# Kernel optimization log

Hardware: AMD Instinct MI355X
Metric: run time of the kernel (lower is better)

## Reference

```python
import jax, jax.numpy as jnp
import numpy as np

ATTN_MULT = 8.0
NEG_INF = float('-inf')

N, Q, S, D = 16, 2048, 2048, 64


def setup_inputs() -> dict:
    key = jax.random.key(0)
    kq, kk, kv, kp = jax.random.split(key, 4)
    return {
        "queries_nqd": jax.random.normal(kq, (N, Q, D), dtype=jnp.float32),
        "keys_nsd": jax.random.normal(kk, (N, S, D), dtype=jnp.float32),
        "values_nsv": jax.random.normal(kv, (N, S, D), dtype=jnp.float32),
        "prefix_len_n": jax.random.randint(kp, (N,), 0, S, dtype=jnp.int64 if jax.config.jax_enable_x64 else jnp.int32),
    }


def reference(queries_nqd, keys_nsd, values_nsv, prefix_len_n):
    # attention_type == 'block_diagonal', backend == 'torch', dropout p == 0
    n, q, d = queries_nqd.shape
    s = keys_nsd.shape[1]
    scale = ATTN_MULT / d
    # prefix-block mask: key position < prefix_len (broadcast over queries)
    block_mask_n1s = (jnp.arange(s)[None, None, :] < prefix_len_n[:, None, None])  # [n,1,s]
    diag_mask_qs = jnp.arange(q)[:, None] == jnp.arange(s)[None, :]                # [q,s]
    mask_nqs = block_mask_n1s | diag_mask_qs[None, :, :]                           # [n,q,s]
    scores_nqs = jnp.einsum('nqd,nsd->nqs', queries_nqd, keys_nsd) * scale
    scores_nqs = jnp.where(mask_nqs, scores_nqs, NEG_INF)
    probs_nqs = jax.nn.softmax(scores_nqs, axis=-1)
    return jnp.einsum('nqs,nsv->nqv', probs_nqs, values_nsv)
```

## Files before the change

### kernel.cpp

```cpp
#include <hip/hip_runtime.h>
#include <hip/hip_bf16.h>
#include <math.h>

#define NH 16
#define QL 2048
#define SL 2048
#define DD 64
#define BQ 128
#define NSPLIT 2
#define PSTR 72
#define QK_SCALE_LOG2E 0.1803368801111f

typedef __attribute__((ext_vector_type(8))) short short8;
typedef __attribute__((ext_vector_type(4))) float floatx4;
typedef __attribute__((ext_vector_type(4))) unsigned short ushort4v;
typedef __attribute__((ext_vector_type(8))) unsigned short ushort8v;

__device__ __forceinline__ unsigned short f2bf(float x) {
    unsigned u = __float_as_uint(x);
    u += 0x7FFFu + ((u >> 16) & 1u);
    return (unsigned short)(u >> 16);
}
__device__ __forceinline__ unsigned int f2bf2u(float x, float y) {
    __hip_bfloat162 h = __float22bfloat162_rn(make_float2(x, y));
    return *(unsigned int*)&h;
}
__device__ __forceinline__ float bf2f(unsigned short h) {
    return __uint_as_float((unsigned)h << 16);
}

__device__ __forceinline__ void gld16(const unsigned short* g, unsigned short* l) {
    __builtin_amdgcn_global_load_lds(
        (const __attribute__((address_space(1))) unsigned int*)g,
        (__attribute__((address_space(3))) unsigned int*)l, 16, 0, 0);
}

__global__ __launch_bounds__(512) void k_prep(
    const float* __restrict__ Kf, const float* __restrict__ Vf,
    unsigned short* __restrict__ Kb, unsigned short* __restrict__ Vtb)
{
    __shared__ unsigned short sT[64][PSTR];
    const int bx = (int)blockIdx.x, tid = (int)threadIdx.x;

    const int gidx = bx * 512 + tid;
    #pragma unroll
    for (int k = 0; k < 2; ++k) {
        int idx = gidx + k * (512 * 512);
        float4 v = ((const float4*)Kf)[idx];
        ushort4v h = { f2bf(v.x), f2bf(v.y), f2bf(v.z), f2bf(v.w) };
        *(ushort4v*)(Kb + (size_t)idx * 4) = h;
    }

    const int n = bx >> 5, s0 = (bx & 31) * 64;
    const float* vb = Vf + ((size_t)n * SL + s0) * DD;
    #pragma unroll
    for (int i = 0; i < 2; ++i) {
        int idx = tid + i * 512;
        int r = idx >> 4, c = (idx & 15) << 2;
        float4 v = *(const float4*)(vb + r * DD + c);
        sT[c + 0][r] = f2bf(v.x);
        sT[c + 1][r] = f2bf(v.y);
        sT[c + 2][r] = f2bf(v.z);
        sT[c + 3][r] = f2bf(v.w);
    }
    __syncthreads();
    const int d = tid >> 3, sg = tid & 7;
    unsigned short* out = Vtb + (size_t)n * DD * SL + (size_t)d * SL + s0 + sg * 8;
    ushort8v a;
    #pragma unroll
    for (int i = 0; i < 8; ++i) a[i] = sT[d][sg * 8 + i];
    *(ushort8v*)out = a;
}

__global__ __launch_bounds__(512, 4) void k_attn(
    const float* __restrict__ Qf, const unsigned short* __restrict__ Kb,
    const unsigned short* __restrict__ Vtb, const int* __restrict__ plen_g,
    unsigned short* __restrict__ Opb, float* __restrict__ Lp)
{
    __shared__ unsigned short sK[4][64 * 64];
    __shared__ unsigned short sVt[4][64 * 64];
    __shared__ unsigned short sP[8 * 16 * 64];

    const int flat = (int)blockIdx.x;
    const int sp   = flat >> 8;
    const int rb   = flat & 255;
    const int n    = (rb + sp) & (NH - 1);
    const int qt   = rb >> 4;
    const int q0   = qt * BQ;
    const int plen = plen_g[n];

    const int tid  = (int)threadIdx.x;
    const int wave = tid >> 6, lane = tid & 63, quad = lane >> 4, l16 = lane & 15;

    const int ptiles = (plen + 63) >> 6;
    const int d0     = q0 >> 6;
    const int tdiag  = d0 + sp;
    const int cnt_p  = (ptiles + 1 - sp) >> 1;
    const int total  = cnt_p + (tdiag >= ptiles ? 1 : 0);

    const int qrow  = wave * 16 + l16;
    const int qglob = q0 + qrow;
    const int pmask = (l16 & 7) * 8;

    const unsigned short* kh = Kb  + (size_t)n * SL * DD;
    const unsigned short* vh = Vtb + (size_t)n * DD * SL;

    const int srow = wave * 8 + (lane >> 3);
    const int scol = ((lane & 7) ^ (srow & 7)) * 8;

    auto tile_of = [&](int i) -> int {
        return (i < cnt_p) ? (sp + (i << 1)) : tdiag;
    };
    auto stage = [&](int t, int b) {
        const unsigned short* kg = kh + ((size_t)t << 6) * DD;
        const unsigned short* vg = vh + (t << 6);
        gld16(kg + srow * DD + scol, sK[b] + wave * 512);
        gld16(vg + (size_t)srow * SL + scol, sVt[b] + wave * 512);
    };

    short8 bQ0, bQ1;
    {
        const float* qf = Qf + ((size_t)(n * QL + qglob)) * DD + quad * 8;
        float4 a0 = *(const float4*)(qf);
        float4 a1 = *(const float4*)(qf + 4);
        float4 c0 = *(const float4*)(qf + 32);
        float4 c1 = *(const float4*)(qf + 36);
        const float S = QK_SCALE_LOG2E;
        unsigned int u0[4] = {
            f2bf2u(a0.x * S, a0.y * S), f2bf2u(a0.z * S, a0.w * S),
            f2bf2u(a1.x * S, a1.y * S), f2bf2u(a1.z * S, a1.w * S) };
        unsigned int u1[4] = {
            f2bf2u(c0.x * S, c0.y * S), f2bf2u(c0.z * S, c0.w * S),
            f2bf2u(c1.x * S, c1.y * S), f2bf2u(c1.z * S, c1.w * S) };
        bQ0 = *(short8*)u0;
        bQ1 = *(short8*)u1;
    }

    stage(tile_of(0), 0);
    if (1 < total) stage(tile_of(1), 1);

    floatx4 acc[4];
    #pragma unroll
    for (int dt = 0; dt < 4; ++dt) acc[dt] = (floatx4){0.f, 0.f, 0.f, 0.f};
    float lsum = 0.f;
    unsigned short* pw = sP + qrow * 64;

    auto do_tile = [&](int t, const unsigned short* sk, const unsigned short* sv) {
        const int s0 = t << 6;

        floatx4 sf[4];
        #pragma unroll
        for (int st2 = 0; st2 < 4; ++st2) sf[st2] = (floatx4){0.f, 0.f, 0.f, 0.f};
        __builtin_amdgcn_s_setprio(1);
        #pragma unroll
        for (int st2 = 0; st2 < 4; ++st2) {
            int krow = st2 * 16 + l16;
            short8 aK0 = *(const short8*)(sk + krow * 64 + (((0 * 4 + quad) ^ (krow & 7)) * 8));
            short8 aK1 = *(const short8*)(sk + krow * 64 + (((1 * 4 + quad) ^ (krow & 7)) * 8));
            sf[st2] = __builtin_amdgcn_mfma_f32_16x16x32_bf16(aK0, bQ0, sf[st2], 0, 0, 0);
            sf[st2] = __builtin_amdgcn_mfma_f32_16x16x32_bf16(aK1, bQ1, sf[st2], 0, 0, 0);
        }
        __builtin_amdgcn_s_setprio(0);

        if (s0 + 64 <= plen) {
            #pragma unroll
            for (int st2 = 0; st2 < 4; ++st2) {
                float p0 = __builtin_amdgcn_exp2f(sf[st2][0]);
                float p1 = __builtin_amdgcn_exp2f(sf[st2][1]);
                float p2 = __builtin_amdgcn_exp2f(sf[st2][2]);
                float p3 = __builtin_amdgcn_exp2f(sf[st2][3]);
                lsum += (p0 + p1) + (p2 + p3);
                uint2 pk = { f2bf2u(p0, p1), f2bf2u(p2, p3) };
                *(uint2*)(pw + ((st2 * 16 + quad * 4) ^ pmask)) = pk;
            }
        } else {
            #pragma unroll
            for (int st2 = 0; st2 < 4; ++st2) {
                float p[4];
                #pragma unroll
                for (int r2 = 0; r2 < 4; ++r2) {
                    int s = s0 + st2 * 16 + quad * 4 + r2;
                    bool valid = (s < plen) || (s == qglob);
                    p[r2] = __builtin_amdgcn_exp2f(valid ? sf[st2][r2] : -INFINITY);
                    lsum += p[r2];
                }
                uint2 pk = { f2bf2u(p[0], p[1]), f2bf2u(p[2], p[3]) };
                *(uint2*)(pw + ((st2 * 16 + quad * 4) ^ pmask)) = pk;
            }
        }

        __builtin_amdgcn_s_setprio(1);
        #pragma unroll
        for (int ks = 0; ks < 2; ++ks) {
            short8 aP = *(const short8*)(pw + ((ks * 32 + quad * 8) ^ pmask));
            #pragma unroll
            for (int dt = 0; dt < 4; ++dt) {
                int vrow = dt * 16 + l16;
                short8 bV = *(const short8*)(sv + vrow * 64 + (((ks * 4 + quad) ^ (vrow & 7)) * 8));
                acc[dt] = __builtin_amdgcn_mfma_f32_16x16x32_bf16(aP, bV, acc[dt], 0, 0, 0);
            }
        }
        __builtin_amdgcn_s_setprio(0);
    };

    const int np = (total + 1) >> 1;
    for (int p = 0; p < np; ++p) {
        asm volatile("s_waitcnt vmcnt(0) lgkmcnt(0)" ::: "memory");
        __builtin_amdgcn_s_barrier();

        const int i0 = 2 * p;
        const int nb = 2 * ((p + 1) & 1);
        if (i0 + 2 < total) stage(tile_of(i0 + 2), nb);
        if (i0 + 3 < total) stage(tile_of(i0 + 3), nb + 1);

        const int cb = 2 * (p & 1);
        do_tile(tile_of(i0), sK[cb], sVt[cb]);
        if (i0 + 1 < total)
            do_tile(tile_of(i0 + 1), sK[cb + 1], sVt[cb + 1]);
    }

    lsum += __shfl_xor(lsum, 16, 64);
    lsum += __shfl_xor(lsum, 32, 64);
    if (quad == 0)
        Lp[((size_t)sp * NH + n) * QL + q0 + qrow] = lsum;

    unsigned short* pws = sP + wave * 16 * 64;
    #pragma unroll
    for (int dt = 0; dt < 4; ++dt) {
        int chunk = dt * 2 + (l16 >> 3);
        #pragma unroll
        for (int r2 = 0; r2 < 4; ++r2) {
            int row = quad * 4 + r2;
            int sw = ((chunk ^ (row & 7)) * 8) + (l16 & 7);
            pws[row * 64 + sw] = f2bf(acc[dt][r2]);
        }
    }
    const size_t qbase = ((size_t)sp * NH + n) * QL + q0 + wave * 16;
    #pragma unroll
    for (int t2 = 0; t2 < 2; ++t2) {
        int row = t2 * 8 + (lane >> 3);
        int chunk = lane & 7;
        int sw = (chunk ^ (row & 7)) * 8;
        ushort8v val = *(const ushort8v*)(pws + row * 64 + sw);
        *(ushort8v*)(Opb + (qbase + row) * DD + chunk * 8) = val;
    }
}

__global__ __launch_bounds__(512) void k_combine(
    const unsigned short* __restrict__ Opb, const float* __restrict__ Lp,
    float* __restrict__ Og)
{
    const int idx = (int)(blockIdx.x * 512 + threadIdx.x);
    const int d8 = idx & 7;
    const int q  = (idx >> 3) & (QL - 1);
    const int n  = idx >> 14;
    float s[8];
    #pragma unroll
    for (int j = 0; j < 8; ++j) s[j] = 0.f;
    float l = 0.f;
    #pragma unroll
    for (int sp = 0; sp < NSPLIT; ++sp) {
        const unsigned short* ob = Opb + (((size_t)sp * NH + n) * QL + q) * DD + d8 * 8;
        ushort8v v = *(const ushort8v*)ob;
        #pragma unroll
        for (int j = 0; j < 8; ++j) s[j] += bf2f(v[j]);
        l += Lp[((size_t)sp * NH + n) * QL + q];
    }
    const float inv = 1.0f / l;
    float4 o0 = { s[0] * inv, s[1] * inv, s[2] * inv, s[3] * inv };
    float4 o1 = { s[4] * inv, s[5] * inv, s[6] * inv, s[7] * inv };
    float* og = Og + ((size_t)n * QL + q) * DD + d8 * 8;
    *(float4*)og = o0;
    *(float4*)(og + 4) = o1;
}

extern "C" void kernel_launch(void* const* d_in, const int* in_sizes, int n_in,
                              void* d_out, int out_size, void* d_ws, size_t ws_size,
                              hipStream_t stream) {
    const float* Qf   = (const float*)d_in[0];
    const float* Kf   = (const float*)d_in[1];
    const float* Vf   = (const float*)d_in[2];
    const int*   plen = (const int*)d_in[3];
    float* Og = (float*)d_out;

    char* ws = (char*)d_ws;
    unsigned short* Kb  = (unsigned short*)(ws);
    unsigned short* Vtb = (unsigned short*)(ws + (4u << 20));
    unsigned short* Opb = (unsigned short*)(ws + (8u << 20));
    float*          Lp  = (float*)(ws + (16u << 20));

    k_prep<<<512, 512, 0, stream>>>(Kf, Vf, Kb, Vtb);
    k_attn<<<NSPLIT * 256, 512, 0, stream>>>(Qf, Kb, Vtb, plen, Opb, Lp);
    k_combine<<<512, 512, 0, stream>>>(Opb, Lp, Og);
}
```

Baseline: 103.6 us.

## Split key tiles four ways, pre-convert Q to bf16, skip empty splits

```diff
diff --git a/kernel.cpp b/kernel.cpp
--- a/kernel.cpp
+++ b/kernel.cpp
@@ -7,7 +7,7 @@
 #define SL 2048
 #define DD 64
 #define BQ 128
-#define NSPLIT 2
+#define NSPLIT 4
 #define PSTR 72
 #define QK_SCALE_LOG2E 0.1803368801111f
 
@@ -36,19 +36,27 @@
 }
 
 __global__ __launch_bounds__(512) void k_prep(
-    const float* __restrict__ Kf, const float* __restrict__ Vf,
-    unsigned short* __restrict__ Kb, unsigned short* __restrict__ Vtb)
+    const float* __restrict__ Qf, const float* __restrict__ Kf, const float* __restrict__ Vf,
+    unsigned short* __restrict__ Qb, unsigned short* __restrict__ Kb, unsigned short* __restrict__ Vtb)
 {
     __shared__ unsigned short sT[64][PSTR];
     const int bx = (int)blockIdx.x, tid = (int)threadIdx.x;
-
     const int gidx = bx * 512 + tid;
+
     #pragma unroll
     for (int k = 0; k < 2; ++k) {
         int idx = gidx + k * (512 * 512);
         float4 v = ((const float4*)Kf)[idx];
         ushort4v h = { f2bf(v.x), f2bf(v.y), f2bf(v.z), f2bf(v.w) };
         *(ushort4v*)(Kb + (size_t)idx * 4) = h;
+    }
+    #pragma unroll
+    for (int k = 0; k < 2; ++k) {
+        int idx = gidx + k * (512 * 512);
+        float4 v = ((const float4*)Qf)[idx];
+        const float S = QK_SCALE_LOG2E;
+        ushort4v h = { f2bf(v.x * S), f2bf(v.y * S), f2bf(v.z * S), f2bf(v.w * S) };
+        *(ushort4v*)(Qb + (size_t)idx * 4) = h;
     }
 
     const int n = bx >> 5, s0 = (bx & 31) * 64;
@@ -73,7 +81,7 @@
 }
 
 __global__ __launch_bounds__(512, 4) void k_attn(
-    const float* __restrict__ Qf, const unsigned short* __restrict__ Kb,
+    const unsigned short* __restrict__ Qb, const unsigned short* __restrict__ Kb,
     const unsigned short* __restrict__ Vtb, const int* __restrict__ plen_g,
     unsigned short* __restrict__ Opb, float* __restrict__ Lp)
 {
@@ -89,14 +97,17 @@
     const int q0   = qt * BQ;
     const int plen = plen_g[n];
 
+    const int ptiles = (plen + 63) >> 6;
+    const int d0     = q0 >> 6;
+    int td = -1;
+    if ((d0 & 3) == sp)            td = d0;
+    else if (((d0 + 1) & 3) == sp) td = d0 + 1;
+    const int cnt_p = (ptiles - sp + 3) >> 2;
+    const int total = cnt_p + ((td >= 0 && td >= ptiles) ? 1 : 0);
+    if (total == 0) return;
+
     const int tid  = (int)threadIdx.x;
     const int wave = tid >> 6, lane = tid & 63, quad = lane >> 4, l16 = lane & 15;
-
-    const int ptiles = (plen + 63) >> 6;
-    const int d0     = q0 >> 6;
-    const int tdiag  = d0 + sp;
-    const int cnt_p  = (ptiles + 1 - sp) >> 1;
-    const int total  = cnt_p + (tdiag >= ptiles ? 1 : 0);
 
     const int qrow  = wave * 16 + l16;
     const int qglob = q0 + qrow;
@@ -109,7 +120,7 @@
     const int scol = ((lane & 7) ^ (srow & 7)) * 8;
 
     auto tile_of = [&](int i) -> int {
-        return (i < cnt_p) ? (sp + (i << 1)) : tdiag;
+        return (i < cnt_p) ? (sp + (i << 2)) : td;
     };
     auto stage = [&](int t, int b) {
         const unsigned short* kg = kh + ((size_t)t << 6) * DD;
@@ -118,23 +129,9 @@
         gld16(vg + (size_t)srow * SL + scol, sVt[b] + wave * 512);
     };
 
-    short8 bQ0, bQ1;
-    {
-        const float* qf = Qf + ((size_t)(n * QL + qglob)) * DD + quad * 8;
-        float4 a0 = *(const float4*)(qf);
-        float4 a1 = *(const float4*)(qf + 4);
-        float4 c0 = *(const float4*)(qf + 32);
-        float4 c1 = *(const float4*)(qf + 36);
-        const float S = QK_SCALE_LOG2E;
-        unsigned int u0[4] = {
-            f2bf2u(a0.x * S, a0.y * S), f2bf2u(a0.z * S, a0.w * S),
-            f2bf2u(a1.x * S, a1.y * S), f2bf2u(a1.z * S, a1.w * S) };
-        unsigned int u1[4] = {
-            f2bf2u(c0.x * S, c0.y * S), f2bf2u(c0.z * S, c0.w * S),
-            f2bf2u(c1.x * S, c1.y * S), f2bf2u(c1.z * S, c1.w * S) };
-        bQ0 = *(short8*)u0;
-        bQ1 = *(short8*)u1;
-    }
+    const unsigned short* qb = Qb + ((size_t)n * QL + qglob) * DD;
+    short8 bQ0 = *(const short8*)(qb + quad * 8);
+    short8 bQ1 = *(const short8*)(qb + 32 + quad * 8);
 
     stage(tile_of(0), 0);
     if (1 < total) stage(tile_of(1), 1);
@@ -248,23 +245,30 @@
 
 __global__ __launch_bounds__(512) void k_combine(
     const unsigned short* __restrict__ Opb, const float* __restrict__ Lp,
-    float* __restrict__ Og)
+    const int* __restrict__ plen_g, float* __restrict__ Og)
 {
     const int idx = (int)(blockIdx.x * 512 + threadIdx.x);
     const int d8 = idx & 7;
     const int q  = (idx >> 3) & (QL - 1);
     const int n  = idx >> 14;
+    const int plen   = plen_g[n];
+    const int ptiles = (plen + 63) >> 6;
+    const int d0     = (q >> 7) << 1;
+    const int dp0    = d0 & 3;
+    const int dp1    = (d0 + 1) & 3;
     float s[8];
     #pragma unroll
     for (int j = 0; j < 8; ++j) s[j] = 0.f;
     float l = 0.f;
     #pragma unroll
     for (int sp = 0; sp < NSPLIT; ++sp) {
-        const unsigned short* ob = Opb + (((size_t)sp * NH + n) * QL + q) * DD + d8 * 8;
-        ushort8v v = *(const ushort8v*)ob;
-        #pragma unroll
-        for (int j = 0; j < 8; ++j) s[j] += bf2f(v[j]);
-        l += Lp[((size_t)sp * NH + n) * QL + q];
+        if ((ptiles > sp) || (sp == dp0) || (sp == dp1)) {
+            const unsigned short* ob = Opb + (((size_t)sp * NH + n) * QL + q) * DD + d8 * 8;
+            ushort8v v = *(const ushort8v*)ob;
+            #pragma unroll
+            for (int j = 0; j < 8; ++j) s[j] += bf2f(v[j]);
+            l += Lp[((size_t)sp * NH + n) * QL + q];
+        }
     }
     const float inv = 1.0f / l;
     float4 o0 = { s[0] * inv, s[1] * inv, s[2] * inv, s[3] * inv };
@@ -286,10 +290,11 @@
     char* ws = (char*)d_ws;
     unsigned short* Kb  = (unsigned short*)(ws);
     unsigned short* Vtb = (unsigned short*)(ws + (4u << 20));
-    unsigned short* Opb = (unsigned short*)(ws + (8u << 20));
-    float*          Lp  = (float*)(ws + (16u << 20));
-
-    k_prep<<<512, 512, 0, stream>>>(Kf, Vf, Kb, Vtb);
-    k_attn<<<NSPLIT * 256, 512, 0, stream>>>(Qf, Kb, Vtb, plen, Opb, Lp);
-    k_combine<<<512, 512, 0, stream>>>(Opb, Lp, Og);
-}
+    unsigned short* Qb  = (unsigned short*)(ws + (8u << 20));
+    unsigned short* Opb = (unsigned short*)(ws + (12u << 20));
+    float*          Lp  = (float*)(ws + (28u << 20));
+
+    k_prep<<<512, 512, 0, stream>>>(Qf, Kf, Vf, Qb, Kb, Vtb);
+    k_attn<<<NSPLIT * 256, 512, 0, stream>>>(Qb, Kb, Vtb, plen, Opb, Lp);
+    k_combine<<<512, 512, 0, stream>>>(Opb, Lp, plen, Og);
+}
```

Result: slower. 106.2 us (+2.5%).
